# Kernel optimization log

Hardware: AMD Instinct MI355X
Metric: run time of the kernel (lower is better)

The kernel has to match this reference:

```python
import jax, jax.numpy as jnp
import numpy as np

N_A, N_P, E = 50000, 50000, 600000
H, D = 8, 16
C = H * D  # hidden_channels = 128
OUT = 16
F_A, F_P = 256, 128
NEG_SLOPE = 0.2
EPS = 1e-5


def setup_inputs():
    key = jax.random.key(0)
    ks = jax.random.split(key, 16)
    return {
        'x_author': jax.random.normal(ks[0], (N_A, F_A), jnp.float32),
        'x_paper': jax.random.normal(ks[1], (N_P, F_P), jnp.float32),
        'W_a': jax.random.normal(ks[2], (F_A, C), jnp.float32) / np.sqrt(F_A).astype(np.float32),
        'b_a': jnp.zeros((C,), jnp.float32),
        'W_p': jax.random.normal(ks[3], (F_P, C), jnp.float32) / np.sqrt(F_P).astype(np.float32),
        'b_p': jnp.zeros((C,), jnp.float32),
        'att_src_ap': jax.random.normal(ks[4], (H, D), jnp.float32) * 0.1,
        'att_dst_ap': jax.random.normal(ks[5], (H, D), jnp.float32) * 0.1,
        'att_src_pp': jax.random.normal(ks[6], (H, D), jnp.float32) * 0.1,
        'att_dst_pp': jax.random.normal(ks[7], (H, D), jnp.float32) * 0.1,
        'k_W': jax.random.normal(ks[8], (C, C), jnp.float32) / np.sqrt(C).astype(np.float32),
        'k_b': jnp.zeros((C,), jnp.float32),
        'q': jax.random.normal(ks[9], (C,), jnp.float32) * 0.1,
        'norm_w': jnp.ones((C,), jnp.float32),
        'norm_b': jnp.zeros((C,), jnp.float32),
        'norm_ms': jnp.ones((C,), jnp.float32),
        'lin_W': jax.random.normal(ks[10], (C, OUT), jnp.float32) / np.sqrt(C).astype(np.float32),
        'lin_b': jnp.zeros((OUT,), jnp.float32),
        'edge_ap': jax.random.randint(ks[11], (2, E), 0, N_A),
        'edge_pp': jax.random.randint(ks[12], (2, E), 0, N_P),
    }


def _edge_type_out(h_src, h_dst, edge, a_src, a_dst, n_dst):
    # Node-level attention for one edge type (PyG HANConv per-metapath GAT).
    alpha_s = jnp.einsum('nhd,hd->nh', h_src, a_src)  # [N_src, H]
    alpha_d = jnp.einsum('nhd,hd->nh', h_dst, a_dst)  # [N_dst, H]
    src, dst = edge[0], edge[1]
    alpha = alpha_s[src] + alpha_d[dst]                       # [E, H]
    alpha = jnp.where(alpha >= 0, alpha, NEG_SLOPE * alpha)   # leaky_relu(0.2)
    m = jax.ops.segment_max(alpha, dst, num_segments=n_dst)
    e = jnp.exp(alpha - m[dst])
    denom = jax.ops.segment_sum(e, dst, num_segments=n_dst)
    attn = e / denom[dst]                                     # softmax over incoming edges
    msg = h_src[src] * attn[:, :, None]                       # [E, H, D]
    out = jax.ops.segment_sum(msg, dst, num_segments=n_dst)   # [n_dst, H, D]
    return jax.nn.relu(out.reshape(n_dst, H * D))


def reference(x_author, x_paper, W_a, b_a, W_p, b_p, att_src_ap, att_dst_ap,
              att_src_pp, att_dst_pp, k_W, k_b, q, norm_w, norm_b, norm_ms,
              lin_W, lin_b, edge_ap, edge_pp):
    # per-node-type projections -> [N, H, D]
    h_a = (x_author @ W_a + b_a).reshape(N_A, H, D)
    h_p = (x_paper @ W_p + b_p).reshape(N_P, H, D)
    # per-edge-type node-level attention + aggregation (both target 'paper')
    out_ap = _edge_type_out(h_a, h_p, edge_ap, att_src_ap, att_dst_ap, N_P)
    out_pp = _edge_type_out(h_p, h_p, edge_pp, att_src_pp, att_dst_pp, N_P)
    # semantic-level attention across the R=2 meta-paths
    outs = jnp.stack([out_ap, out_pp], axis=0)               # [R, N_P, C]
    w = jnp.tanh(outs @ k_W + k_b).mean(axis=1) @ q          # [R]
    beta = jax.nn.softmax(w)
    out = jnp.einsum('rnc,r->nc', outs, beta)                # [N_P, C]
    # GraphNorm (single graph: stats over all nodes)
    mean = out.mean(axis=0)
    o = out - mean * norm_ms
    var = (o * o).mean(axis=0)
    o = norm_w * o / jnp.sqrt(var + EPS) + norm_b
    # final classifier
    return o @ lin_W + lin_b
```

## Files before the change

kernel.cpp:

```cpp
#include <hip/hip_runtime.h>
#include <math.h>

#define NN   50000
#define EE   600000
#define CCH  128
#define HH   8
#define DD   16
#define OUTC 16
#define NEG  0.2f
#define EPSN 1e-5f
#define SLICE_DIV 12500

typedef _Float16 f16x8 __attribute__((ext_vector_type(8)));
typedef float    f32x4 __attribute__((ext_vector_type(4)));

__device__ __forceinline__ float fast_tanh(float x) {
    x = fminf(10.f, fmaxf(-10.f, x));
    float e = __expf(2.f * x);
    return (e - 1.f) / (e + 1.f);
}

__global__ __launch_bounds__(256) void prep_k(const float* __restrict__ W_a,
        const float* __restrict__ W_p, const float* __restrict__ k_W,
        const float* __restrict__ lin_W, const int* __restrict__ ea,
        const int* __restrict__ ep, _Float16* __restrict__ Wt_a,
        _Float16* __restrict__ Wt_p, _Float16* __restrict__ kWt,
        _Float16* __restrict__ linWt, int* __restrict__ counts)
{
    int b = blockIdx.x;
    if (b < 264) {
        int id = b * 256 + threadIdx.x;
        if (id < 32768) {
            int k = id >> 7, n = id & 127;
            Wt_a[n * 256 + k] = (_Float16)W_a[id];
        } else if (id < 49152) {
            int i = id - 32768; int k = i >> 7, n = i & 127;
            Wt_p[n * 128 + k] = (_Float16)W_p[i];
        } else if (id < 65536) {
            int i = id - 49152; int k = i >> 7, n = i & 127;
            kWt[n * 128 + k] = (_Float16)k_W[i];
        } else if (id < 67584) {
            int i = id - 65536; int k = i >> 4, n = i & 15;
            linWt[n * 128 + k] = (_Float16)lin_W[i];
        }
    } else {
        int bb = b - 264;
        int slice = bb & 7;
        int chunk = bb >> 3;
        int lo = slice * SLICE_DIV, hi = lo + SLICE_DIV;
        int base = chunk * 1024;
#pragma unroll
        for (int it = 0; it < 4; ++it) {
            int e = base + it * 256 + threadIdx.x;
            if (e < EE) {
                int d = ea[EE + e];
                if (d >= lo && d < hi) atomicAdd(&counts[d], 1);
            } else if (e < 2 * EE) {
                int d = NN + ep[e];
                if (d >= lo && d < hi) atomicAdd(&counts[d], 1);
            }
        }
    }
}

__global__ __launch_bounds__(256) void gemm2_k(const float* __restrict__ X_a,
        const float* __restrict__ X_p, const _Float16* __restrict__ Wt_a,
        const _Float16* __restrict__ Wt_p, const float* __restrict__ b_a,
        const float* __restrict__ b_p,
        const float* __restrict__ att_s_ap, const float* __restrict__ att_d_ap,
        const float* __restrict__ att_s_pp, const float* __restrict__ att_d_pp,
        _Float16* __restrict__ h_a, _Float16* __restrict__ h_p,
        float* __restrict__ as_ap, float* __restrict__ ad_ap,
        float* __restrict__ as_pp, float* __restrict__ ad_pp, int GBn)
{
    __shared__ _Float16 As[64][40];
    __shared__ _Float16 Bs[128][40];
    const int which = ((int)blockIdx.x >= GBn) ? 1 : 0;
    const float* X = which ? X_p : X_a;
    const _Float16* Wt = which ? Wt_p : Wt_a;
    const float* bias = which ? b_p : b_a;
    _Float16* Y = which ? h_p : h_a;
    const int K = which ? 128 : 256;
    const int t = threadIdx.x;
    const int r0 = (blockIdx.x - which * GBn) * 64;
    const int lane = t & 63;
    const int wv = t >> 6;
    const int m16 = lane & 15;
    const int kq = lane >> 4;
    f32x4 acc[8];
#pragma unroll
    for (int i = 0; i < 8; ++i) acc[i] = (f32x4){0.f, 0.f, 0.f, 0.f};

    const int ar = t >> 2;
    const int ak = (t & 3) * 8;
    const int br = t >> 1;
    const int bk = (t & 1) * 16;

    for (int kc = 0; kc < K; kc += 32) {
        int row = r0 + ar;
        f16x8 av;
        if (row < NN) {
            const float4* gp = (const float4*)&X[row * K + kc + ak];
            float4 x0 = gp[0], x1 = gp[1];
            av[0] = (_Float16)x0.x; av[1] = (_Float16)x0.y;
            av[2] = (_Float16)x0.z; av[3] = (_Float16)x0.w;
            av[4] = (_Float16)x1.x; av[5] = (_Float16)x1.y;
            av[6] = (_Float16)x1.z; av[7] = (_Float16)x1.w;
        } else {
#pragma unroll
            for (int j = 0; j < 8; ++j) av[j] = (_Float16)0.f;
        }
        *(f16x8*)&As[ar][ak] = av;
        const f16x8* wp = (const f16x8*)&Wt[br * K + kc + bk];
        *(f16x8*)&Bs[br][bk]     = wp[0];
        *(f16x8*)&Bs[br][bk + 8] = wp[1];
        __syncthreads();
        f16x8 af = *(const f16x8*)&As[wv * 16 + m16][kq * 8];
#pragma unroll
        for (int i = 0; i < 8; ++i) {
            f16x8 bf = *(const f16x8*)&Bs[i * 16 + m16][kq * 8];
            acc[i] = __builtin_amdgcn_mfma_f32_16x16x32_f16(af, bf, acc[i], 0, 0, 0);
        }
        __syncthreads();
    }
    const int rbase = r0 + wv * 16 + kq * 4;
#pragma unroll
    for (int i = 0; i < 8; ++i) {
        int col = i * 16 + m16;
        float b = bias[col];
        float hv[4];
#pragma unroll
        for (int rr = 0; rr < 4; ++rr) hv[rr] = acc[i][rr] + b;
#pragma unroll
        for (int rr = 0; rr < 4; ++rr)
            if (rbase + rr < NN) Y[(rbase + rr) * 128 + col] = (_Float16)hv[rr];
        if (which == 0) {
            float av = att_s_ap[i * 16 + m16];
            float p[4];
#pragma unroll
            for (int rr = 0; rr < 4; ++rr) p[rr] = hv[rr] * av;
#pragma unroll
            for (int x = 1; x < 16; x <<= 1)
#pragma unroll
                for (int rr = 0; rr < 4; ++rr) p[rr] += __shfl_xor(p[rr], x, 64);
            if (m16 == 0) {
#pragma unroll
                for (int rr = 0; rr < 4; ++rr)
                    if (rbase + rr < NN) as_ap[(rbase + rr) * 8 + i] = p[rr];
            }
        } else {
            float a1 = att_d_ap[i * 16 + m16];
            float a2 = att_s_pp[i * 16 + m16];
            float a3 = att_d_pp[i * 16 + m16];
            float p1[4], p2[4], p3[4];
#pragma unroll
            for (int rr = 0; rr < 4; ++rr) {
                p1[rr] = hv[rr] * a1; p2[rr] = hv[rr] * a2; p3[rr] = hv[rr] * a3;
            }
#pragma unroll
            for (int x = 1; x < 16; x <<= 1) {
#pragma unroll
                for (int rr = 0; rr < 4; ++rr) {
                    p1[rr] += __shfl_xor(p1[rr], x, 64);
                    p2[rr] += __shfl_xor(p2[rr], x, 64);
                    p3[rr] += __shfl_xor(p3[rr], x, 64);
                }
            }
            if (m16 == 0) {
#pragma unroll
                for (int rr = 0; rr < 4; ++rr) {
                    if (rbase + rr < NN) {
                        ad_ap[(rbase + rr) * 8 + i] = p1[rr];
                        as_pp[(rbase + rr) * 8 + i] = p2[rr];
                        ad_pp[(rbase + rr) * 8 + i] = p3[rr];
                    }
                }
            }
        }
    }
}

__global__ __launch_bounds__(256) void scan1_k(const int* __restrict__ counts,
        int* __restrict__ incl, int* __restrict__ bsum) {
    __shared__ int s[256];
    int t = threadIdx.x;
    int i = blockIdx.x * 256 + t;
    int v = (i < 2 * NN) ? counts[i] : 0;
    s[t] = v; __syncthreads();
    for (int off = 1; off < 256; off <<= 1) {
        int x = (t >= off) ? s[t - off] : 0;
        __syncthreads();
        s[t] += x;
        __syncthreads();
    }
    incl[i] = s[t];
    if (t == 255) bsum[blockIdx.x] = s[255];
}

__global__ __launch_bounds__(512) void scan2_k(int* __restrict__ bsum, int nb) {
    __shared__ int s[512];
    int t = threadIdx.x;
    int v = (t < nb) ? bsum[t] : 0;
    s[t] = v; __syncthreads();
    for (int off = 1; off < 512; off <<= 1) {
        int x = (t >= off) ? s[t - off] : 0;
        __syncthreads();
        s[t] += x;
        __syncthreads();
    }
    if (t < nb) bsum[t] = s[t] - v;
}

__global__ __launch_bounds__(256) void scan3_k(const int* __restrict__ incl,
        const int* __restrict__ bexcl, int* __restrict__ rp) {
    int i = blockIdx.x * 256 + threadIdx.x;
    if (i < 2 * NN) rp[i + 1] = incl[i] + bexcl[blockIdx.x];
    if (i == 0) rp[0] = 0;
}

__global__ __launch_bounds__(256) void scat_k(const int* __restrict__ ea,
        const int* __restrict__ ep, const int* __restrict__ rp,
        int* __restrict__ fill, int* __restrict__ csr)
{
    int bb = blockIdx.x;
    int slice = bb & 7;
    int chunk = bb >> 3;
    int lo = slice * SLICE_DIV, hi = lo + SLICE_DIV;
    int base = chunk * 1024;
#pragma unroll
    for (int it = 0; it < 4; ++it) {
        int e = base + it * 256 + threadIdx.x;
        if (e < EE) {
            int d = ea[EE + e];
            if (d >= lo && d < hi) {
                int pos = rp[d] + atomicAdd(&fill[d], 1);
                csr[pos] = ea[e];
            }
        } else if (e < 2 * EE) {
            int d = NN + ep[e];
            if (d >= lo && d < hi) {
                int pos = rp[d] + atomicAdd(&fill[d], 1);
                csr[pos] = ep[e - EE];
            }
        }
    }
}

__global__ __launch_bounds__(256) void agg4_k(
        const _Float16* __restrict__ h_a, const _Float16* __restrict__ h_p,
        const float* __restrict__ as_ap, const float* __restrict__ ad_ap,
        const float* __restrict__ as_pp, const float* __restrict__ ad_pp,
        const int* __restrict__ rp, const int* __restrict__ csr,
        _Float16* __restrict__ out_ap, _Float16* __restrict__ out_pp)
{
    int wave = threadIdx.x >> 6;
    int lane = threadIdx.x & 63;
    int q = lane >> 4;
    int sub = lane & 15;
    int gnode = blockIdx.x * 16 + wave * 4 + q;
    bool pp = gnode >= NN;
    int n = pp ? gnode - NN : gnode;
    const _Float16* hsrc = pp ? h_p : h_a;
    const float* as = pp ? as_pp : as_ap;
    const float* ad = pp ? ad_pp : ad_ap;
    _Float16* outb = pp ? out_pp : out_ap;
    int h = sub >> 1;
    float adv = ad[n * 8 + h];
    int p = rp[gnode], p1 = rp[gnode + 1];
    float l = 0.f;
    float acc[8] = {0.f, 0.f, 0.f, 0.f, 0.f, 0.f, 0.f, 0.f};
    for (; p + 1 < p1; p += 2) {
        int s0 = csr[p], s1 = csr[p + 1];
        float a0 = as[s0 * 8 + h] + adv;
        float a1 = as[s1 * 8 + h] + adv;
        a0 = (a0 >= 0.f) ? a0 : NEG * a0;
        a1 = (a1 >= 0.f) ? a1 : NEG * a1;
        float w0 = __expf(a0);
        float w1 = __expf(a1);
        f16x8 v0 = *(const f16x8*)&hsrc[s0 * CCH + sub * 8];
        f16x8 v1 = *(const f16x8*)&hsrc[s1 * CCH + sub * 8];
        l += w0 + w1;
#pragma unroll
        for (int i = 0; i < 8; ++i) acc[i] += w0 * (float)v0[i] + w1 * (float)v1[i];
    }
    if (p < p1) {
        int s0 = csr[p];
        float a0 = as[s0 * 8 + h] + adv;
        a0 = (a0 >= 0.f) ? a0 : NEG * a0;
        float w0 = __expf(a0);
        f16x8 v0 = *(const f16x8*)&hsrc[s0 * CCH + sub * 8];
        l += w0;
#pragma unroll
        for (int i = 0; i < 8; ++i) acc[i] += w0 * (float)v0[i];
    }
    float inv = (l > 0.f) ? 1.f / l : 0.f;
    f16x8 o;
#pragma unroll
    for (int i = 0; i < 8; ++i) o[i] = (_Float16)fmaxf(acc[i] * inv, 0.f);
    *(f16x8*)&outb[n * CCH + sub * 8] = o;
}

__global__ __launch_bounds__(256) void stats2_k(const _Float16* __restrict__ Xa,
        const _Float16* __restrict__ Xb,
        float* __restrict__ sA, float* __restrict__ sB,
        float* __restrict__ ssA, float* __restrict__ ssB, float* __restrict__ sAB)
{
    __shared__ float sbuf[640];
    int t = threadIdx.x;
    for (int i = t; i < 640; i += 256) sbuf[i] = 0.f;
    __syncthreads();
    int oct = t & 15, rs = t >> 4;
    int start = (int)blockIdx.x * 196;
    int end = start + 196; if (end > NN) end = NN;
    float sa[8] = {0,0,0,0,0,0,0,0}, sb[8] = {0,0,0,0,0,0,0,0};
    float ssa[8] = {0,0,0,0,0,0,0,0}, ssb[8] = {0,0,0,0,0,0,0,0};
    float sab[8] = {0,0,0,0,0,0,0,0};
    for (int r = start + rs; r < end; r += 16) {
        f16x8 va = *(const f16x8*)&Xa[r * 128 + oct * 8];
        f16x8 vb = *(const f16x8*)&Xb[r * 128 + oct * 8];
#pragma unroll
        for (int j = 0; j < 8; ++j) {
            float a = (float)va[j], b = (float)vb[j];
            sa[j] += a; sb[j] += b;
            ssa[j] += a * a; ssb[j] += b * b; sab[j] += a * b;
        }
    }
#pragma unroll
    for (int x = 16; x < 64; x <<= 1) {
#pragma unroll
        for (int j = 0; j < 8; ++j) {
            sa[j]  += __shfl_xor(sa[j],  x, 64);
            sb[j]  += __shfl_xor(sb[j],  x, 64);
            ssa[j] += __shfl_xor(ssa[j], x, 64);
            ssb[j] += __shfl_xor(ssb[j], x, 64);
            sab[j] += __shfl_xor(sab[j], x, 64);
        }
    }
    if ((t & 63) < 16) {
        int c0 = oct * 8;
#pragma unroll
        for (int j = 0; j < 8; ++j) {
            atomicAdd(&sbuf[c0 + j], sa[j]);
            atomicAdd(&sbuf[128 + c0 + j], sb[j]);
            atomicAdd(&sbuf[256 + c0 + j], ssa[j]);
            atomicAdd(&sbuf[384 + c0 + j], ssb[j]);
            atomicAdd(&sbuf[512 + c0 + j], sab[j]);
        }
    }
    __syncthreads();
    if (t < 128) {
        atomicAdd(&sA[t],  sbuf[t]);
        atomicAdd(&sB[t],  sbuf[128 + t]);
        atomicAdd(&ssA[t], sbuf[256 + t]);
        atomicAdd(&ssB[t], sbuf[384 + t]);
        atomicAdd(&sAB[t], sbuf[512 + t]);
    }
}

__global__ __launch_bounds__(256) void sem2_k(const _Float16* __restrict__ Xa,
        const _Float16* __restrict__ Xb, const _Float16* __restrict__ kWt,
        const float* __restrict__ kb, const float* __restrict__ q,
        float* __restrict__ wacc, int GBn)
{
    __shared__ float wred[4];
    const int b = (int)blockIdx.x;
    const int which = (b >= GBn) ? 1 : 0;
    const _Float16* Xh = which ? Xb : Xa;
    const int r0 = (b - which * GBn) * 64;
    const int t = threadIdx.x;
    const int lane = t & 63, wv = t >> 6;
    const int m16 = lane & 15, kq = lane >> 4;
    const int arow = r0 + wv * 16 + m16;
    f16x8 af[4];
    if (arow < NN) {
#pragma unroll
        for (int kc4 = 0; kc4 < 4; ++kc4)
            af[kc4] = *(const f16x8*)&Xh[arow * 128 + kc4 * 32 + kq * 8];
    } else {
#pragma unroll
        for (int kc4 = 0; kc4 < 4; ++kc4)
#pragma unroll
            for (int j = 0; j < 8; ++j) af[kc4][j] = (_Float16)0.f;
    }
    f32x4 acc[8];
#pragma unroll
    for (int i = 0; i < 8; ++i) acc[i] = (f32x4){0.f, 0.f, 0.f, 0.f};
#pragma unroll
    for (int kc4 = 0; kc4 < 4; ++kc4) {
#pragma unroll
        for (int i = 0; i < 8; ++i) {
            f16x8 bf = *(const f16x8*)&kWt[(i * 16 + m16) * 128 + kc4 * 32 + kq * 8];
            acc[i] = __builtin_amdgcn_mfma_f32_16x16x32_f16(af[kc4], bf, acc[i], 0, 0, 0);
        }
    }
    const int rbase = r0 + wv * 16 + kq * 4;
    float local = 0.f;
#pragma unroll
    for (int i = 0; i < 8; ++i) {
        float kbc = kb[i * 16 + m16], qc = q[i * 16 + m16];
#pragma unroll
        for (int rr = 0; rr < 4; ++rr)
            if (rbase + rr < NN) local += fast_tanh(acc[i][rr] + kbc) * qc;
    }
#pragma unroll
    for (int x = 1; x < 64; x <<= 1) local += __shfl_xor(local, x, 64);
    if (lane == 0) wred[wv] = local;
    __syncthreads();
    if (t == 0) {
        float s = wred[0] + wred[1] + wred[2] + wred[3];
        atomicAdd(&wacc[which * 256 + (b & 15) * 16], s);
    }
}

__global__ __launch_bounds__(256) void final2_k(
        const _Float16* __restrict__ oa, const _Float16* __restrict__ ob,
        const float* __restrict__ wacc,
        const float* __restrict__ sA, const float* __restrict__ sB,
        const float* __restrict__ ssA, const float* __restrict__ ssB,
        const float* __restrict__ sAB,
        const float* __restrict__ ms, const float* __restrict__ nw,
        const float* __restrict__ nb,
        const _Float16* __restrict__ linWt, const float* __restrict__ linb,
        float* __restrict__ out)
{
    __shared__ _Float16 As[64][136];
    __shared__ float scl[128], shf[128];
    __shared__ float bcoef[2];
    int t = threadIdx.x;
    if (t < 128) {
        float w0s = 0.f, w1s = 0.f;
#pragma unroll
        for (int i = 0; i < 16; ++i) {
            w0s += wacc[i * 16];
            w1s += wacc[256 + i * 16];
        }
        float w0 = w0s * (1.f / NN), w1 = w1s * (1.f / NN);
        float mm = fmaxf(w0, w1);
        float e0 = __expf(w0 - mm), e1 = __expf(w1 - mm);
        float b0 = e0 / (e0 + e1), b1 = e1 / (e0 + e1);
        if (t == 0) { bcoef[0] = b0; bcoef[1] = b1; }
        int c = t;
        float mean = (b0 * sA[c] + b1 * sB[c]) * (1.f / NN);
        float ex2 = (b0 * b0 * ssA[c] + 2.f * b0 * b1 * sAB[c] + b1 * b1 * ssB[c]) * (1.f / NN);
        float a = mean * ms[c];
        float var = ex2 - 2.f * a * mean + a * a;
        float sc = nw[c] * rsqrtf(var + EPSN);
        scl[c] = sc;
        shf[c] = nb[c] - a * sc;
    }
    __syncthreads();
    float b0 = bcoef[0], b1 = bcoef[1];
    int r0 = blockIdx.x * 64;
    int row = t >> 2, cp = (t & 3) * 32;
    int gr = r0 + row;
    if (gr < NN) {
#pragma unroll
        for (int i = 0; i < 4; ++i) {
            int c0 = cp + i * 8;
            f16x8 va = *(const f16x8*)&oa[gr * CCH + c0];
            f16x8 vb = *(const f16x8*)&ob[gr * CCH + c0];
            f16x8 o;
#pragma unroll
            for (int e2 = 0; e2 < 8; ++e2) {
                float v = b0 * (float)va[e2] + b1 * (float)vb[e2];
                o[e2] = (_Float16)(v * scl[c0 + e2] + shf[c0 + e2]);
            }
            *(f16x8*)&As[row][c0] = o;
        }
    } else {
        f16x8 z;
#pragma unroll
        for (int e2 = 0; e2 < 8; ++e2) z[e2] = (_Float16)0.f;
#pragma unroll
        for (int i = 0; i < 4; ++i) *(f16x8*)&As[row][cp + i * 8] = z;
    }
    __syncthreads();
    int lane = t & 63, wv = t >> 6;
    int m16 = lane & 15, kq = lane >> 4;
    f32x4 acc = (f32x4){0.f, 0.f, 0.f, 0.f};
#pragma unroll
    for (int kc = 0; kc < 128; kc += 32) {
        f16x8 af = *(const f16x8*)&As[wv * 16 + m16][kc + kq * 8];
        f16x8 bf = *(const f16x8*)&linWt[m16 * 128 + kc + kq * 8];
        acc = __builtin_amdgcn_mfma_f32_16x16x32_f16(af, bf, acc, 0, 0, 0);
    }
    float lb = linb[m16];
#pragma unroll
    for (int r = 0; r < 4; ++r) {
        int gr2 = r0 + wv * 16 + kq * 4 + r;
        if (gr2 < NN) out[gr2 * 16 + m16] = acc[r] + lb;
    }
}

extern "C" void kernel_launch(void* const* d_in, const int* in_sizes, int n_in,
                              void* d_out, int out_size, void* d_ws, size_t ws_size,
                              hipStream_t stream) {
    const float* x_a   = (const float*)d_in[0];
    const float* x_p   = (const float*)d_in[1];
    const float* W_a   = (const float*)d_in[2];
    const float* b_a   = (const float*)d_in[3];
    const float* W_p   = (const float*)d_in[4];
    const float* b_p   = (const float*)d_in[5];
    const float* att_src_ap = (const float*)d_in[6];
    const float* att_dst_ap = (const float*)d_in[7];
    const float* att_src_pp = (const float*)d_in[8];
    const float* att_dst_pp = (const float*)d_in[9];
    const float* k_W   = (const float*)d_in[10];
    const float* k_b   = (const float*)d_in[11];
    const float* q     = (const float*)d_in[12];
    const float* norm_w = (const float*)d_in[13];
    const float* norm_b = (const float*)d_in[14];
    const float* norm_ms = (const float*)d_in[15];
    const float* lin_W = (const float*)d_in[16];
    const float* lin_b = (const float*)d_in[17];
    const int* edge_ap = (const int*)d_in[18];
    const int* edge_pp = (const int*)d_in[19];
    float* out = (float*)d_out;

    char* base = (char*)d_ws;
    size_t off = 0;
    auto alloc = [&](size_t bytes) -> void* {
        void* r = base + off;
        off += (bytes + 255) & ~(size_t)255;
        return r;
    };
    _Float16* h_a    = (_Float16*)alloc((size_t)NN * CCH * 2);
    _Float16* h_p    = (_Float16*)alloc((size_t)NN * CCH * 2);
    _Float16* out_ap = (_Float16*)alloc((size_t)NN * CCH * 2);
    _Float16* out_pp = (_Float16*)alloc((size_t)NN * CCH * 2);
    float* as_ap  = (float*)alloc((size_t)NN * HH * 4);
    float* ad_ap  = (float*)alloc((size_t)NN * HH * 4);
    float* as_pp  = (float*)alloc((size_t)NN * HH * 4);
    float* ad_pp  = (float*)alloc((size_t)NN * HH * 4);
    _Float16* Wt_a = (_Float16*)alloc((size_t)128 * 256 * 2);
    _Float16* Wt_p = (_Float16*)alloc((size_t)128 * 128 * 2);
    _Float16* kWt  = (_Float16*)alloc((size_t)128 * 128 * 2);
    _Float16* linWt = (_Float16*)alloc((size_t)16 * 128 * 2);
    int* incl    = (int*)alloc((size_t)100352 * 4);
    int* bsum    = (int*)alloc(512 * 4);
    int* rp_all  = (int*)alloc((size_t)(2 * NN + 1) * 4);
    int* csr_all = (int*)alloc((size_t)2 * EE * 4);
    const size_t ZCOUNT = 100000 + 100000 + 512 + 5 * 128;
    int* zz = (int*)alloc(ZCOUNT * 4);
    int* counts = zz;
    int* fill   = zz + 100000;
    float* wacc = (float*)(zz + 200000);
    float* sA   = (float*)(zz + 200512);
    float* sB   = sA + 128;
    float* ssA  = sB + 128;
    float* ssB  = ssA + 128;
    float* sAB  = ssB + 128;

    (void)in_sizes; (void)n_in; (void)out_size; (void)ws_size;

    hipMemsetAsync(zz, 0, ZCOUNT * 4, stream);

    const int CHUNKS = (2 * EE + 1023) / 1024;
    prep_k<<<264 + CHUNKS * 8, 256, 0, stream>>>(W_a, W_p, k_W, lin_W, edge_ap, edge_pp,
                                                 Wt_a, Wt_p, kWt, linWt, counts);

    const int GB = (NN + 63) / 64;
    gemm2_k<<<2 * GB, 256, 0, stream>>>(x_a, x_p, Wt_a, Wt_p, b_a, b_p,
                                        att_src_ap, att_dst_ap, att_src_pp, att_dst_pp,
                                        h_a, h_p, as_ap, ad_ap, as_pp, ad_pp, GB);

    const int SB = 392;
    scan1_k<<<SB, 256, 0, stream>>>(counts, incl, bsum);
    scan2_k<<<1, 512, 0, stream>>>(bsum, SB);
    scan3_k<<<SB, 256, 0, stream>>>(incl, bsum, rp_all);

    scat_k<<<CHUNKS * 8, 256, 0, stream>>>(edge_ap, edge_pp, rp_all, fill, csr_all);

    agg4_k<<<2 * NN / 16, 256, 0, stream>>>(h_a, h_p, as_ap, ad_ap, as_pp, ad_pp,
                                            rp_all, csr_all, out_ap, out_pp);

    stats2_k<<<256, 256, 0, stream>>>(out_ap, out_pp, sA, sB, ssA, ssB, sAB);

    sem2_k<<<2 * GB, 256, 0, stream>>>(out_ap, out_pp, kWt, k_b, q, wacc, GB);

    final2_k<<<GB, 256, 0, stream>>>(out_ap, out_pp, wacc, sA, sB, ssA, ssB, sAB,
                                     norm_ms, norm_w, norm_b, linWt, lin_b, out);
}
```

Baseline: 403.1 us.

## Widen GEMM K-chunk, unroll aggregation by four, merge stats and semantic kernels

The projection GEMM now stages 64-wide K chunks in shared memory, halving the number of sync barriers per tile at the cost of more LDS per block. The edge aggregation loop processes four neighbours per iteration to increase memory-level parallelism for the gathers. The GraphNorm statistics kernel and the semantic attention kernel are merged into one launch, with block index selecting the role, removing a launch and letting both run concurrently.

Measured after the change: 393.9 us. -2.3%, faster.

```diff
diff --git a/kernel.cpp b/kernel.cpp
--- a/kernel.cpp
+++ b/kernel.cpp
@@ -73,8 +73,8 @@
         float* __restrict__ as_ap, float* __restrict__ ad_ap,
         float* __restrict__ as_pp, float* __restrict__ ad_pp, int GBn)
 {
-    __shared__ _Float16 As[64][40];
-    __shared__ _Float16 Bs[128][40];
+    __shared__ _Float16 As[64][72];
+    __shared__ _Float16 Bs[128][72];
     const int which = ((int)blockIdx.x >= GBn) ? 1 : 0;
     const float* X = which ? X_p : X_a;
     const _Float16* Wt = which ? Wt_p : Wt_a;
@@ -92,34 +92,44 @@
     for (int i = 0; i < 8; ++i) acc[i] = (f32x4){0.f, 0.f, 0.f, 0.f};
 
     const int ar = t >> 2;
-    const int ak = (t & 3) * 8;
+    const int aks = (t & 3) * 16;
     const int br = t >> 1;
-    const int bk = (t & 1) * 16;
-
-    for (int kc = 0; kc < K; kc += 32) {
+    const int bks = (t & 1) * 32;
+
+    for (int kc = 0; kc < K; kc += 64) {
         int row = r0 + ar;
-        f16x8 av;
+        f16x8 av0, av1;
         if (row < NN) {
-            const float4* gp = (const float4*)&X[row * K + kc + ak];
-            float4 x0 = gp[0], x1 = gp[1];
-            av[0] = (_Float16)x0.x; av[1] = (_Float16)x0.y;
-            av[2] = (_Float16)x0.z; av[3] = (_Float16)x0.w;
-            av[4] = (_Float16)x1.x; av[5] = (_Float16)x1.y;
-            av[6] = (_Float16)x1.z; av[7] = (_Float16)x1.w;
+            const float4* gp = (const float4*)&X[row * K + kc + aks];
+            float4 x0 = gp[0], x1 = gp[1], x2 = gp[2], x3 = gp[3];
+            av0[0] = (_Float16)x0.x; av0[1] = (_Float16)x0.y;
+            av0[2] = (_Float16)x0.z; av0[3] = (_Float16)x0.w;
+            av0[4] = (_Float16)x1.x; av0[5] = (_Float16)x1.y;
+            av0[6] = (_Float16)x1.z; av0[7] = (_Float16)x1.w;
+            av1[0] = (_Float16)x2.x; av1[1] = (_Float16)x2.y;
+            av1[2] = (_Float16)x2.z; av1[3] = (_Float16)x2.w;
+            av1[4] = (_Float16)x3.x; av1[5] = (_Float16)x3.y;
+            av1[6] = (_Float16)x3.z; av1[7] = (_Float16)x3.w;
         } else {
 #pragma unroll
-            for (int j = 0; j < 8; ++j) av[j] = (_Float16)0.f;
-        }
-        *(f16x8*)&As[ar][ak] = av;
-        const f16x8* wp = (const f16x8*)&Wt[br * K + kc + bk];
-        *(f16x8*)&Bs[br][bk]     = wp[0];
-        *(f16x8*)&Bs[br][bk + 8] = wp[1];
-        __syncthreads();
-        f16x8 af = *(const f16x8*)&As[wv * 16 + m16][kq * 8];
+            for (int j = 0; j < 8; ++j) { av0[j] = (_Float16)0.f; av1[j] = (_Float16)0.f; }
+        }
+        *(f16x8*)&As[ar][aks]     = av0;
+        *(f16x8*)&As[ar][aks + 8] = av1;
+        const f16x8* wp = (const f16x8*)&Wt[br * K + kc + bks];
+        *(f16x8*)&Bs[br][bks]      = wp[0];
+        *(f16x8*)&Bs[br][bks + 8]  = wp[1];
+        *(f16x8*)&Bs[br][bks + 16] = wp[2];
+        *(f16x8*)&Bs[br][bks + 24] = wp[3];
+        __syncthreads();
+        f16x8 afa = *(const f16x8*)&As[wv * 16 + m16][kq * 8];
+        f16x8 afb = *(const f16x8*)&As[wv * 16 + m16][32 + kq * 8];
 #pragma unroll
         for (int i = 0; i < 8; ++i) {
-            f16x8 bf = *(const f16x8*)&Bs[i * 16 + m16][kq * 8];
-            acc[i] = __builtin_amdgcn_mfma_f32_16x16x32_f16(af, bf, acc[i], 0, 0, 0);
+            f16x8 bfa = *(const f16x8*)&Bs[i * 16 + m16][kq * 8];
+            acc[i] = __builtin_amdgcn_mfma_f32_16x16x32_f16(afa, bfa, acc[i], 0, 0, 0);
+            f16x8 bfb = *(const f16x8*)&Bs[i * 16 + m16][32 + kq * 8];
+            acc[i] = __builtin_amdgcn_mfma_f32_16x16x32_f16(afb, bfb, acc[i], 0, 0, 0);
         }
         __syncthreads();
     }
@@ -269,21 +279,28 @@
     int p = rp[gnode], p1 = rp[gnode + 1];
     float l = 0.f;
     float acc[8] = {0.f, 0.f, 0.f, 0.f, 0.f, 0.f, 0.f, 0.f};
-    for (; p + 1 < p1; p += 2) {
-        int s0 = csr[p], s1 = csr[p + 1];
+    for (; p + 3 < p1; p += 4) {
+        int s0 = csr[p], s1 = csr[p + 1], s2 = csr[p + 2], s3 = csr[p + 3];
         float a0 = as[s0 * 8 + h] + adv;
         float a1 = as[s1 * 8 + h] + adv;
+        float a2 = as[s2 * 8 + h] + adv;
+        float a3 = as[s3 * 8 + h] + adv;
         a0 = (a0 >= 0.f) ? a0 : NEG * a0;
         a1 = (a1 >= 0.f) ? a1 : NEG * a1;
-        float w0 = __expf(a0);
-        float w1 = __expf(a1);
+        a2 = (a2 >= 0.f) ? a2 : NEG * a2;
+        a3 = (a3 >= 0.f) ? a3 : NEG * a3;
+        float w0 = __expf(a0), w1 = __expf(a1), w2 = __expf(a2), w3 = __expf(a3);
         f16x8 v0 = *(const f16x8*)&hsrc[s0 * CCH + sub * 8];
         f16x8 v1 = *(const f16x8*)&hsrc[s1 * CCH + sub * 8];
-        l += w0 + w1;
-#pragma unroll
-        for (int i = 0; i < 8; ++i) acc[i] += w0 * (float)v0[i] + w1 * (float)v1[i];
-    }
-    if (p < p1) {
+        f16x8 v2 = *(const f16x8*)&hsrc[s2 * CCH + sub * 8];
+        f16x8 v3 = *(const f16x8*)&hsrc[s3 * CCH + sub * 8];
+        l += (w0 + w1) + (w2 + w3);
+#pragma unroll
+        for (int i = 0; i < 8; ++i)
+            acc[i] += (w0 * (float)v0[i] + w1 * (float)v1[i])
+                    + (w2 * (float)v2[i] + w3 * (float)v3[i]);
+    }
+    for (; p < p1; ++p) {
         int s0 = csr[p];
         float a0 = as[s0 * 8 + h] + adv;
         a0 = (a0 >= 0.f) ? a0 : NEG * a0;
@@ -300,115 +317,111 @@
     *(f16x8*)&outb[n * CCH + sub * 8] = o;
 }
 
-__global__ __launch_bounds__(256) void stats2_k(const _Float16* __restrict__ Xa,
-        const _Float16* __restrict__ Xb,
-        float* __restrict__ sA, float* __restrict__ sB,
-        float* __restrict__ ssA, float* __restrict__ ssB, float* __restrict__ sAB)
+__global__ __launch_bounds__(256) void semstats2_k(const _Float16* __restrict__ Xa,
+        const _Float16* __restrict__ Xb, const _Float16* __restrict__ kWt,
+        const float* __restrict__ kb, const float* __restrict__ q,
+        float* __restrict__ wacc, float* __restrict__ sA, float* __restrict__ sB,
+        float* __restrict__ ssA, float* __restrict__ ssB, float* __restrict__ sAB,
+        int GBn)
 {
     __shared__ float sbuf[640];
-    int t = threadIdx.x;
-    for (int i = t; i < 640; i += 256) sbuf[i] = 0.f;
-    __syncthreads();
-    int oct = t & 15, rs = t >> 4;
-    int start = (int)blockIdx.x * 196;
-    int end = start + 196; if (end > NN) end = NN;
-    float sa[8] = {0,0,0,0,0,0,0,0}, sb[8] = {0,0,0,0,0,0,0,0};
-    float ssa[8] = {0,0,0,0,0,0,0,0}, ssb[8] = {0,0,0,0,0,0,0,0};
-    float sab[8] = {0,0,0,0,0,0,0,0};
-    for (int r = start + rs; r < end; r += 16) {
-        f16x8 va = *(const f16x8*)&Xa[r * 128 + oct * 8];
-        f16x8 vb = *(const f16x8*)&Xb[r * 128 + oct * 8];
-#pragma unroll
-        for (int j = 0; j < 8; ++j) {
-            float a = (float)va[j], b = (float)vb[j];
-            sa[j] += a; sb[j] += b;
-            ssa[j] += a * a; ssb[j] += b * b; sab[j] += a * b;
-        }
-    }
-#pragma unroll
-    for (int x = 16; x < 64; x <<= 1) {
-#pragma unroll
-        for (int j = 0; j < 8; ++j) {
-            sa[j]  += __shfl_xor(sa[j],  x, 64);
-            sb[j]  += __shfl_xor(sb[j],  x, 64);
-            ssa[j] += __shfl_xor(ssa[j], x, 64);
-            ssb[j] += __shfl_xor(ssb[j], x, 64);
-            sab[j] += __shfl_xor(sab[j], x, 64);
-        }
-    }
-    if ((t & 63) < 16) {
-        int c0 = oct * 8;
-#pragma unroll
-        for (int j = 0; j < 8; ++j) {
-            atomicAdd(&sbuf[c0 + j], sa[j]);
-            atomicAdd(&sbuf[128 + c0 + j], sb[j]);
-            atomicAdd(&sbuf[256 + c0 + j], ssa[j]);
-            atomicAdd(&sbuf[384 + c0 + j], ssb[j]);
-            atomicAdd(&sbuf[512 + c0 + j], sab[j]);
-        }
-    }
-    __syncthreads();
-    if (t < 128) {
-        atomicAdd(&sA[t],  sbuf[t]);
-        atomicAdd(&sB[t],  sbuf[128 + t]);
-        atomicAdd(&ssA[t], sbuf[256 + t]);
-        atomicAdd(&ssB[t], sbuf[384 + t]);
-        atomicAdd(&sAB[t], sbuf[512 + t]);
-    }
-}
-
-__global__ __launch_bounds__(256) void sem2_k(const _Float16* __restrict__ Xa,
-        const _Float16* __restrict__ Xb, const _Float16* __restrict__ kWt,
-        const float* __restrict__ kb, const float* __restrict__ q,
-        float* __restrict__ wacc, int GBn)
-{
-    __shared__ float wred[4];
-    const int b = (int)blockIdx.x;
-    const int which = (b >= GBn) ? 1 : 0;
-    const _Float16* Xh = which ? Xb : Xa;
-    const int r0 = (b - which * GBn) * 64;
     const int t = threadIdx.x;
-    const int lane = t & 63, wv = t >> 6;
-    const int m16 = lane & 15, kq = lane >> 4;
-    const int arow = r0 + wv * 16 + m16;
-    f16x8 af[4];
-    if (arow < NN) {
-#pragma unroll
-        for (int kc4 = 0; kc4 < 4; ++kc4)
-            af[kc4] = *(const f16x8*)&Xh[arow * 128 + kc4 * 32 + kq * 8];
+    if ((int)blockIdx.x < 256) {
+        for (int i = t; i < 640; i += 256) sbuf[i] = 0.f;
+        __syncthreads();
+        int oct = t & 15, rs = t >> 4;
+        int start = (int)blockIdx.x * 196;
+        int end = start + 196; if (end > NN) end = NN;
+        float sa[8] = {0,0,0,0,0,0,0,0}, sb[8] = {0,0,0,0,0,0,0,0};
+        float ssa[8] = {0,0,0,0,0,0,0,0}, ssb[8] = {0,0,0,0,0,0,0,0};
+        float sab[8] = {0,0,0,0,0,0,0,0};
+        for (int r = start + rs; r < end; r += 16) {
+            f16x8 va = *(const f16x8*)&Xa[r * 128 + oct * 8];
+            f16x8 vb = *(const f16x8*)&Xb[r * 128 + oct * 8];
+#pragma unroll
+            for (int j = 0; j < 8; ++j) {
+                float a = (float)va[j], b = (float)vb[j];
+                sa[j] += a; sb[j] += b;
+                ssa[j] += a * a; ssb[j] += b * b; sab[j] += a * b;
+            }
+        }
+#pragma unroll
+        for (int x = 16; x < 64; x <<= 1) {
+#pragma unroll
+            for (int j = 0; j < 8; ++j) {
+                sa[j]  += __shfl_xor(sa[j],  x, 64);
+                sb[j]  += __shfl_xor(sb[j],  x, 64);
+                ssa[j] += __shfl_xor(ssa[j], x, 64);
+                ssb[j] += __shfl_xor(ssb[j], x, 64);
+                sab[j] += __shfl_xor(sab[j], x, 64);
+            }
+        }
+        if ((t & 63) < 16) {
+            int c0 = oct * 8;
+#pragma unroll
+            for (int j = 0; j < 8; ++j) {
+                atomicAdd(&sbuf[c0 + j], sa[j]);
+                atomicAdd(&sbuf[128 + c0 + j], sb[j]);
+                atomicAdd(&sbuf[256 + c0 + j], ssa[j]);
+                atomicAdd(&sbuf[384 + c0 + j], ssb[j]);
+                atomicAdd(&sbuf[512 + c0 + j], sab[j]);
+            }
+        }
+        __syncthreads();
+        if (t < 128) {
+            atomicAdd(&sA[t],  sbuf[t]);
+            atomicAdd(&sB[t],  sbuf[128 + t]);
+            atomicAdd(&ssA[t], sbuf[256 + t]);
+            atomicAdd(&ssB[t], sbuf[384 + t]);
+            atomicAdd(&sAB[t], sbuf[512 + t]);
+        }
     } else {
-#pragma unroll
-        for (int kc4 = 0; kc4 < 4; ++kc4)
-#pragma unroll
-            for (int j = 0; j < 8; ++j) af[kc4][j] = (_Float16)0.f;
-    }
-    f32x4 acc[8];
-#pragma unroll
-    for (int i = 0; i < 8; ++i) acc[i] = (f32x4){0.f, 0.f, 0.f, 0.f};
-#pragma unroll
-    for (int kc4 = 0; kc4 < 4; ++kc4) {
+        const int b = (int)blockIdx.x - 256;
+        const int which = (b >= GBn) ? 1 : 0;
+        const _Float16* Xh = which ? Xb : Xa;
+        const int r0 = (b - which * GBn) * 64;
+        const int lane = t & 63, wv = t >> 6;
+        const int m16 = lane & 15, kq = lane >> 4;
+        const int arow = r0 + wv * 16 + m16;
+        f16x8 af[4];
+        if (arow < NN) {
+#pragma unroll
+            for (int kc4 = 0; kc4 < 4; ++kc4)
+                af[kc4] = *(const f16x8*)&Xh[arow * 128 + kc4 * 32 + kq * 8];
+        } else {
+#pragma unroll
+            for (int kc4 = 0; kc4 < 4; ++kc4)
+#pragma unroll
+                for (int j = 0; j < 8; ++j) af[kc4][j] = (_Float16)0.f;
+        }
+        f32x4 acc[8];
+#pragma unroll
+        for (int i = 0; i < 8; ++i) acc[i] = (f32x4){0.f, 0.f, 0.f, 0.f};
+#pragma unroll
+        for (int kc4 = 0; kc4 < 4; ++kc4) {
+#pragma unroll
+            for (int i = 0; i < 8; ++i) {
+                f16x8 bf = *(const f16x8*)&kWt[(i * 16 + m16) * 128 + kc4 * 32 + kq * 8];
+                acc[i] = __builtin_amdgcn_mfma_f32_16x16x32_f16(af[kc4], bf, acc[i], 0, 0, 0);
+            }
+        }
+        const int rbase = r0 + wv * 16 + kq * 4;
+        float local = 0.f;
 #pragma unroll
         for (int i = 0; i < 8; ++i) {
-            f16x8 bf = *(const f16x8*)&kWt[(i * 16 + m16) * 128 + kc4 * 32 + kq * 8];
-            acc[i] = __builtin_amdgcn_mfma_f32_16x16x32_f16(af[kc4], bf, acc[i], 0, 0, 0);
-        }
-    }
-    const int rbase = r0 + wv * 16 + kq * 4;
-    float local = 0.f;
-#pragma unroll
-    for (int i = 0; i < 8; ++i) {
-        float kbc = kb[i * 16 + m16], qc = q[i * 16 + m16];
-#pragma unroll
-        for (int rr = 0; rr < 4; ++rr)
-            if (rbase + rr < NN) local += fast_tanh(acc[i][rr] + kbc) * qc;
-    }
-#pragma unroll
-    for (int x = 1; x < 64; x <<= 1) local += __shfl_xor(local, x, 64);
-    if (lane == 0) wred[wv] = local;
-    __syncthreads();
-    if (t == 0) {
-        float s = wred[0] + wred[1] + wred[2] + wred[3];
-        atomicAdd(&wacc[which * 256 + (b & 15) * 16], s);
+            float kbc = kb[i * 16 + m16], qc = q[i * 16 + m16];
+#pragma unroll
+            for (int rr = 0; rr < 4; ++rr)
+                if (rbase + rr < NN) local += fast_tanh(acc[i][rr] + kbc) * qc;
+        }
+#pragma unroll
+        for (int x = 1; x < 64; x <<= 1) local += __shfl_xor(local, x, 64);
+        if (lane == 0) sbuf[wv] = local;
+        __syncthreads();
+        if (t == 0) {
+            float s = sbuf[0] + sbuf[1] + sbuf[2] + sbuf[3];
+            atomicAdd(&wacc[which * 256 + (b & 15) * 16], s);
+        }
     }
 }
 
@@ -574,9 +587,8 @@
     agg4_k<<<2 * NN / 16, 256, 0, stream>>>(h_a, h_p, as_ap, ad_ap, as_pp, ad_pp,
                                             rp_all, csr_all, out_ap, out_pp);
 
-    stats2_k<<<256, 256, 0, stream>>>(out_ap, out_pp, sA, sB, ssA, ssB, sAB);
-
-    sem2_k<<<2 * GB, 256, 0, stream>>>(out_ap, out_pp, kWt, k_b, q, wacc, GB);
+    semstats2_k<<<256 + 2 * GB, 256, 0, stream>>>(out_ap, out_pp, kWt, k_b, q, wacc,
+                                                  sA, sB, ssA, ssB, sAB, GB);
 
     final2_k<<<GB, 256, 0, stream>>>(out_ap, out_pp, wacc, sA, sB, ssA, ssB, sAB,
                                      norm_ms, norm_w, norm_b, linWt, lin_b, out);
```
